# Kernel optimization log

Hardware: AMD Instinct MI355X
Metric: run time of the kernel (lower is better)

## Reference

```python
import jax, jax.numpy as jnp
import numpy as np

EPS_BALL = 1e-5  # Poincare-ball projection margin


def project_to_ball(x):
    # clip vectors to lie strictly inside the unit ball (norm <= 1 - eps)
    norm = jnp.linalg.norm(x, axis=-1, keepdims=True)
    maxnorm = 1.0 - EPS_BALL
    scale = jnp.where(norm > maxnorm, maxnorm / jnp.maximum(norm, 1e-12), 1.0)
    return x * scale


def setup_inputs() -> dict:
    key = jax.random.key(0)
    k1, k2, k3, k4, k5 = jax.random.split(key, 5)
    N, D, M, B = 200000, 256, 200000, 512
    embeddings = jax.random.normal(k1, (N, D), dtype=jnp.float32)
    member_indices = jax.random.randint(k2, (M,), 0, N)
    segment_ids = jnp.sort(jax.random.randint(k3, (M,), 0, B))
    tc = jax.random.normal(k4, (B, D), dtype=jnp.float32)
    teacher_centroids = tc / jnp.maximum(jnp.linalg.norm(tc, axis=-1, keepdims=True), 1e-12)
    teacher_cohesion = jax.random.uniform(k5, (B,), dtype=jnp.float32) * 0.2
    return {
        "embeddings": embeddings,
        "teacher_centroids": teacher_centroids,
        "teacher_cohesion": teacher_cohesion,
        "member_indices": member_indices,
        "segment_ids": segment_ids,
        "num_segments": B,
    }


def reference(embeddings, teacher_centroids, teacher_cohesion, member_indices, segment_ids, num_segments):
    projected = project_to_ball(embeddings)
    norms = jnp.maximum(jnp.linalg.norm(projected, axis=-1, keepdims=True), 1e-8)
    directions = projected / norms                       # [N, D] unit directions

    members = directions[member_indices]                 # [M, D] ragged gather
    seg_sum = jax.ops.segment_sum(members, segment_ids, num_segments=num_segments)  # [B, D]
    counts = jax.ops.segment_sum(jnp.ones((members.shape[0],), members.dtype),
                                 segment_ids, num_segments=num_segments)            # [B]
    mean_raw = seg_sum / jnp.maximum(counts, 1.0)[:, None]                          # per-branch mean
    centroid = mean_raw / jnp.maximum(jnp.linalg.norm(mean_raw, axis=-1, keepdims=True), 1e-12)

    # 1 - <centroid, teacher_centroid> per branch
    centroid_losses = 1.0 - jnp.sum(centroid * teacher_centroids, axis=-1)          # [B]
    # mean_b(<m, centroid>) == <mean_raw, centroid>, so cohesion = 1 - that dot
    cohesion = 1.0 - jnp.sum(mean_raw * centroid, axis=-1)                          # [B]
    cohesion_losses = jax.nn.relu(cohesion - teacher_cohesion)
    return centroid_losses.mean() + cohesion_losses.mean()
```

## Files before the change

kernel.cpp:

```cpp
#include <hip/hip_runtime.h>
#include <hip/hip_bf16.h>


constexpr int D = 256;
constexpr int CHUNK = 32;
constexpr float MAXNORM = 1.0f - 1e-5f;

__device__ __forceinline__ float wave_reduce_add(float v) {
    #pragma unroll
    for (int off = 32; off >= 1; off >>= 1)
        v += __shfl_xor(v, off, 64);
    return v;
}

__global__ void __launch_bounds__(256)
gather_accum_kernel(const float* __restrict__ emb,
                    const int*   __restrict__ midx,
                    const int*   __restrict__ segid,
                    float* __restrict__ seg_sum,
                    float* __restrict__ counts,
                    int M) {
    const int wave = blockIdx.x * (blockDim.x >> 6) + (threadIdx.x >> 6);
    const int lane = threadIdx.x & 63;
    int m = wave * CHUNK;
    if (m >= M) return;
    const int mend = min(m + CHUNK, M);

    float4 acc = {0.f, 0.f, 0.f, 0.f};
    float  cnt = 0.f;
    int cur_seg = segid[m];

    while (m < mend) {
        if (m + 4 <= mend && segid[m + 3] == cur_seg) {
            const int i0 = midx[m + 0], i1 = midx[m + 1], i2 = midx[m + 2], i3 = midx[m + 3];
            const float4 v0 = *reinterpret_cast<const float4*>(emb + (size_t)i0 * D + lane * 4);
            const float4 v1 = *reinterpret_cast<const float4*>(emb + (size_t)i1 * D + lane * 4);
            const float4 v2 = *reinterpret_cast<const float4*>(emb + (size_t)i2 * D + lane * 4);
            const float4 v3 = *reinterpret_cast<const float4*>(emb + (size_t)i3 * D + lane * 4);
            float s[4];
            s[0] = v0.x * v0.x + v0.y * v0.y + v0.z * v0.z + v0.w * v0.w;
            s[1] = v1.x * v1.x + v1.y * v1.y + v1.z * v1.z + v1.w * v1.w;
            s[2] = v2.x * v2.x + v2.y * v2.y + v2.z * v2.z + v2.w * v2.w;
            s[3] = v3.x * v3.x + v3.y * v3.y + v3.z * v3.z + v3.w * v3.w;
            #pragma unroll
            for (int off = 32; off >= 1; off >>= 1) {
                #pragma unroll
                for (int j = 0; j < 4; ++j)
                    s[j] += __shfl_xor(s[j], off, 64);
            }
            float f[4];
            #pragma unroll
            for (int j = 0; j < 4; ++j) {
                const float norm  = sqrtf(s[j]);
                const float scale = (norm > MAXNORM) ? (MAXNORM / fmaxf(norm, 1e-12f)) : 1.0f;
                f[j] = scale / fmaxf(norm * scale, 1e-8f);
            }
            acc.x += v0.x * f[0] + v1.x * f[1] + v2.x * f[2] + v3.x * f[3];
            acc.y += v0.y * f[0] + v1.y * f[1] + v2.y * f[2] + v3.y * f[3];
            acc.z += v0.z * f[0] + v1.z * f[1] + v2.z * f[2] + v3.z * f[3];
            acc.w += v0.w * f[0] + v1.w * f[1] + v2.w * f[2] + v3.w * f[3];
            cnt += 4.f;
            m += 4;
        } else {
            const int seg = segid[m];
            if (seg != cur_seg) {
                float* dst = seg_sum + (size_t)cur_seg * D + lane * 4;
                atomicAdd(dst + 0, acc.x);
                atomicAdd(dst + 1, acc.y);
                atomicAdd(dst + 2, acc.z);
                atomicAdd(dst + 3, acc.w);
                if (lane == 0) atomicAdd(&counts[cur_seg], cnt);
                acc = {0.f, 0.f, 0.f, 0.f};
                cnt = 0.f;
                cur_seg = seg;
            }
            const int idx = midx[m];
            const float4 v = *reinterpret_cast<const float4*>(emb + (size_t)idx * D + lane * 4);
            float ss = v.x * v.x + v.y * v.y + v.z * v.z + v.w * v.w;
            ss = wave_reduce_add(ss);
            const float norm  = sqrtf(ss);
            const float scale = (norm > MAXNORM) ? (MAXNORM / fmaxf(norm, 1e-12f)) : 1.0f;
            const float f     = scale / fmaxf(norm * scale, 1e-8f);
            acc.x += v.x * f;
            acc.y += v.y * f;
            acc.z += v.z * f;
            acc.w += v.w * f;
            cnt += 1.f;
            m += 1;
        }
    }
    float* dst = seg_sum + (size_t)cur_seg * D + lane * 4;
    atomicAdd(dst + 0, acc.x);
    atomicAdd(dst + 1, acc.y);
    atomicAdd(dst + 2, acc.z);
    atomicAdd(dst + 3, acc.w);
    if (lane == 0) atomicAdd(&counts[cur_seg], cnt);
}

__global__ void __launch_bounds__(256)
finalize_kernel(const float* __restrict__ seg_sum,
                const float* __restrict__ counts,
                const float* __restrict__ tcent,
                const float* __restrict__ tcoh,
                float* __restrict__ out,
                int B) {
    const int seg  = blockIdx.x * (blockDim.x >> 6) + (threadIdx.x >> 6);
    const int lane = threadIdx.x & 63;
    if (seg >= B) return;

    const float4 s = *reinterpret_cast<const float4*>(seg_sum + (size_t)seg * D + lane * 4);
    const float  c = fmaxf(counts[seg], 1.0f);
    const float inv_c = 1.0f / c;
    float4 mean = {s.x * inv_c, s.y * inv_c, s.z * inv_c, s.w * inv_c};

    float ss = mean.x * mean.x + mean.y * mean.y + mean.z * mean.z + mean.w * mean.w;
    ss = wave_reduce_add(ss);
    const float mnorm = sqrtf(ss);
    const float inv   = 1.0f / fmaxf(mnorm, 1e-12f);

    const float4 t = *reinterpret_cast<const float4*>(tcent + (size_t)seg * D + lane * 4);
    float dt = mean.x * t.x + mean.y * t.y + mean.z * t.z + mean.w * t.w;
    dt = wave_reduce_add(dt) * inv;

    const float centroid_loss = 1.0f - dt;
    const float cohesion      = 1.0f - ss * inv;
    const float coh_loss      = fmaxf(cohesion - tcoh[seg], 0.0f);

    if (lane == 0)
        atomicAdd(out, (centroid_loss + coh_loss) / (float)B);
}

extern "C" void kernel_launch(void* const* d_in, const int* in_sizes, int n_in,
                              void* d_out, int out_size, void* d_ws, size_t ws_size,
                              hipStream_t stream) {
    const float* emb   = (const float*)d_in[0];
    const float* tcent = (const float*)d_in[1];
    const float* tcoh  = (const float*)d_in[2];
    const int*   midx  = (const int*)d_in[3];
    const int*   segid = (const int*)d_in[4];
    const int B = in_sizes[2];
    const int M = in_sizes[3];

    float* seg_sum = (float*)d_ws;
    float* counts  = seg_sum + (size_t)B * D;

    hipMemsetAsync(d_ws, 0, ((size_t)B * D + B) * sizeof(float), stream);
    hipMemsetAsync(d_out, 0, sizeof(float), stream);

    const int waves_per_block = 4;
    const int n_waves = (M + CHUNK - 1) / CHUNK;
    const int blocks  = (n_waves + waves_per_block - 1) / waves_per_block;
    gather_accum_kernel<<<blocks, 256, 0, stream>>>(emb, midx, segid, seg_sum, counts, M);

    const int blocks2 = (B + waves_per_block - 1) / waves_per_block;
    finalize_kernel<<<blocks2, 256, 0, stream>>>(seg_sum, counts, tcent, tcoh, (float*)d_out, B);
}
```

Baseline: 305.7 us.

## Precompute per-row direction factors in a separate pass and widen gather unroll

Adds a row_norm_kernel that streams every embedding row once and stores a per-row scale factor (ball projection plus normalisation). The gather kernel then multiplies each gathered row by its stored factor instead of doing a cross-lane shuffle reduction per member, and its fast path now batches 8 members instead of 4. This removes the shuffle and reduction latency from the gather loop and allows more loads in flight per wave. The cost is an extra full read of the embedding table (all N rows, not only the gathered ones), which may or may not be partly served from the large last-level cache on the later gather.

```diff
diff --git a/kernel.cpp b/kernel.cpp
--- a/kernel.cpp
+++ b/kernel.cpp
@@ -13,8 +13,55 @@
     return v;
 }
 
+__device__ __forceinline__ float dir_factor(float ss) {
+    const float norm  = sqrtf(ss);
+    const float scale = (norm > MAXNORM) ? (MAXNORM / fmaxf(norm, 1e-12f)) : 1.0f;
+    return scale / fmaxf(norm * scale, 1e-8f);
+}
+
+__global__ void __launch_bounds__(256)
+row_norm_kernel(const float* __restrict__ emb,
+                float* __restrict__ fvec,
+                int N) {
+    const int wave = blockIdx.x * (blockDim.x >> 6) + (threadIdx.x >> 6);
+    const int lane = threadIdx.x & 63;
+    const int r0 = wave * 4;
+    if (r0 >= N) return;
+
+    if (r0 + 4 <= N) {
+        const float4 v0 = *reinterpret_cast<const float4*>(emb + (size_t)(r0 + 0) * D + lane * 4);
+        const float4 v1 = *reinterpret_cast<const float4*>(emb + (size_t)(r0 + 1) * D + lane * 4);
+        const float4 v2 = *reinterpret_cast<const float4*>(emb + (size_t)(r0 + 2) * D + lane * 4);
+        const float4 v3 = *reinterpret_cast<const float4*>(emb + (size_t)(r0 + 3) * D + lane * 4);
+        float s[4];
+        s[0] = v0.x * v0.x + v0.y * v0.y + v0.z * v0.z + v0.w * v0.w;
+        s[1] = v1.x * v1.x + v1.y * v1.y + v1.z * v1.z + v1.w * v1.w;
+        s[2] = v2.x * v2.x + v2.y * v2.y + v2.z * v2.z + v2.w * v2.w;
+        s[3] = v3.x * v3.x + v3.y * v3.y + v3.z * v3.z + v3.w * v3.w;
+        #pragma unroll
+        for (int off = 32; off >= 1; off >>= 1) {
+            #pragma unroll
+            for (int j = 0; j < 4; ++j)
+                s[j] += __shfl_xor(s[j], off, 64);
+        }
+        if (lane == 0) {
+            float4 f4 = make_float4(dir_factor(s[0]), dir_factor(s[1]),
+                                    dir_factor(s[2]), dir_factor(s[3]));
+            *reinterpret_cast<float4*>(fvec + r0) = f4;
+        }
+    } else {
+        for (int r = r0; r < N; ++r) {
+            const float4 v = *reinterpret_cast<const float4*>(emb + (size_t)r * D + lane * 4);
+            float ss = v.x * v.x + v.y * v.y + v.z * v.z + v.w * v.w;
+            ss = wave_reduce_add(ss);
+            if (lane == 0) fvec[r] = dir_factor(ss);
+        }
+    }
+}
+
 __global__ void __launch_bounds__(256)
 gather_accum_kernel(const float* __restrict__ emb,
+                    const float* __restrict__ fvec,
                     const int*   __restrict__ midx,
                     const int*   __restrict__ segid,
                     float* __restrict__ seg_sum,
@@ -31,36 +78,26 @@
     int cur_seg = segid[m];
 
     while (m < mend) {
-        if (m + 4 <= mend && segid[m + 3] == cur_seg) {
-            const int i0 = midx[m + 0], i1 = midx[m + 1], i2 = midx[m + 2], i3 = midx[m + 3];
-            const float4 v0 = *reinterpret_cast<const float4*>(emb + (size_t)i0 * D + lane * 4);
-            const float4 v1 = *reinterpret_cast<const float4*>(emb + (size_t)i1 * D + lane * 4);
-            const float4 v2 = *reinterpret_cast<const float4*>(emb + (size_t)i2 * D + lane * 4);
-            const float4 v3 = *reinterpret_cast<const float4*>(emb + (size_t)i3 * D + lane * 4);
-            float s[4];
-            s[0] = v0.x * v0.x + v0.y * v0.y + v0.z * v0.z + v0.w * v0.w;
-            s[1] = v1.x * v1.x + v1.y * v1.y + v1.z * v1.z + v1.w * v1.w;
-            s[2] = v2.x * v2.x + v2.y * v2.y + v2.z * v2.z + v2.w * v2.w;
-            s[3] = v3.x * v3.x + v3.y * v3.y + v3.z * v3.z + v3.w * v3.w;
+        if (m + 8 <= mend && segid[m + 7] == cur_seg) {
+            int   idx[8];
+            float ff[8];
             #pragma unroll
-            for (int off = 32; off >= 1; off >>= 1) {
-                #pragma unroll
-                for (int j = 0; j < 4; ++j)
-                    s[j] += __shfl_xor(s[j], off, 64);
+            for (int j = 0; j < 8; ++j) idx[j] = midx[m + j];
+            #pragma unroll
+            for (int j = 0; j < 8; ++j) ff[j] = fvec[idx[j]];
+            float4 v[8];
+            #pragma unroll
+            for (int j = 0; j < 8; ++j)
+                v[j] = *reinterpret_cast<const float4*>(emb + (size_t)idx[j] * D + lane * 4);
+            #pragma unroll
+            for (int j = 0; j < 8; ++j) {
+                acc.x += v[j].x * ff[j];
+                acc.y += v[j].y * ff[j];
+                acc.z += v[j].z * ff[j];
+                acc.w += v[j].w * ff[j];
             }
-            float f[4];
-            #pragma unroll
-            for (int j = 0; j < 4; ++j) {
-                const float norm  = sqrtf(s[j]);
-                const float scale = (norm > MAXNORM) ? (MAXNORM / fmaxf(norm, 1e-12f)) : 1.0f;
-                f[j] = scale / fmaxf(norm * scale, 1e-8f);
-            }
-            acc.x += v0.x * f[0] + v1.x * f[1] + v2.x * f[2] + v3.x * f[3];
-            acc.y += v0.y * f[0] + v1.y * f[1] + v2.y * f[2] + v3.y * f[3];
-            acc.z += v0.z * f[0] + v1.z * f[1] + v2.z * f[2] + v3.z * f[3];
-            acc.w += v0.w * f[0] + v1.w * f[1] + v2.w * f[2] + v3.w * f[3];
-            cnt += 4.f;
-            m += 4;
+            cnt += 8.f;
+            m += 8;
         } else {
             const int seg = segid[m];
             if (seg != cur_seg) {
@@ -75,12 +112,8 @@
                 cur_seg = seg;
             }
             const int idx = midx[m];
+            const float f = fvec[idx];
             const float4 v = *reinterpret_cast<const float4*>(emb + (size_t)idx * D + lane * 4);
-            float ss = v.x * v.x + v.y * v.y + v.z * v.z + v.w * v.w;
-            ss = wave_reduce_add(ss);
-            const float norm  = sqrtf(ss);
-            const float scale = (norm > MAXNORM) ? (MAXNORM / fmaxf(norm, 1e-12f)) : 1.0f;
-            const float f     = scale / fmaxf(norm * scale, 1e-8f);
             acc.x += v.x * f;
             acc.y += v.y * f;
             acc.z += v.z * f;
@@ -140,18 +173,25 @@
     const int*   segid = (const int*)d_in[4];
     const int B = in_sizes[2];
     const int M = in_sizes[3];
+    const int N = in_sizes[0] / D;
 
     float* seg_sum = (float*)d_ws;
     float* counts  = seg_sum + (size_t)B * D;
+    float* fvec    = counts + B;
 
     hipMemsetAsync(d_ws, 0, ((size_t)B * D + B) * sizeof(float), stream);
     hipMemsetAsync(d_out, 0, sizeof(float), stream);
 
     const int waves_per_block = 4;
-    const int n_waves = (M + CHUNK - 1) / CHUNK;
-    const int blocks  = (n_waves + waves_per_block - 1) / waves_per_block;
-    gather_accum_kernel<<<blocks, 256, 0, stream>>>(emb, midx, segid, seg_sum, counts, M);
 
-    const int blocks2 = (B + waves_per_block - 1) / waves_per_block;
-    finalize_kernel<<<blocks2, 256, 0, stream>>>(seg_sum, counts, tcent, tcoh, (float*)d_out, B);
+    const int n_waves1 = (N + 3) / 4;
+    const int blocks1  = (n_waves1 + waves_per_block - 1) / waves_per_block;
+    row_norm_kernel<<<blocks1, 256, 0, stream>>>(emb, fvec, N);
+
+    const int n_waves2 = (M + CHUNK - 1) / CHUNK;
+    const int blocks2  = (n_waves2 + waves_per_block - 1) / waves_per_block;
+    gather_accum_kernel<<<blocks2, 256, 0, stream>>>(emb, fvec, midx, segid, seg_sum, counts, M);
+
+    const int blocks3 = (B + waves_per_block - 1) / waves_per_block;
+    finalize_kernel<<<blocks3, 256, 0, stream>>>(seg_sum, counts, tcent, tcoh, (float*)d_out, B);
 }
```

Result: slower. 346.5 us (+13.3%).
